# Performance work log

Measured on AMD Instinct MI355X. Metric: run time of the kernel, lower is better.

The kernel has to match this reference:

```python
import jax, jax.numpy as jnp
import numpy as np

NODE_DIM = 64
HIDDEN_DIM = 128
N_NODES = 100000
N_EDGES = 1000000


def setup_inputs() -> dict:
    key = jax.random.key(0)
    ks = jax.random.split(key, 9)
    node_rep = jax.random.normal(ks[0], (N_NODES, NODE_DIM), dtype=jnp.float32)
    edge_index = jax.random.randint(ks[1], (2, N_EDGES), 0, N_NODES, dtype=jnp.int64)
    s = 0.02  # init std (n_layers scale omitted; values irrelevant for math)
    W1 = jax.random.normal(ks[2], (2 * NODE_DIM, HIDDEN_DIM), dtype=jnp.float32) * s
    b1 = jnp.zeros((HIDDEN_DIM,), dtype=jnp.float32)
    W2 = jax.random.normal(ks[3], (HIDDEN_DIM, HIDDEN_DIM), dtype=jnp.float32) * s
    b2 = jnp.zeros((HIDDEN_DIM,), dtype=jnp.float32)
    W3 = jax.random.normal(ks[4], (HIDDEN_DIM, 1), dtype=jnp.float32) * s
    b3 = jnp.zeros((1,), dtype=jnp.float32)
    return {"node_rep": node_rep, "edge_index": edge_index,
            "W1": W1, "b1": b1, "W2": W2, "b2": b2, "W3": W3, "b3": b3}


def reference(node_rep, edge_index, W1, b1, W2, b2, W3, b3):
    # gather src/dst node reps per edge: [E, node_dim] each
    src = node_rep[edge_index[0]]
    dst = node_rep[edge_index[1]]
    feat = jnp.concatenate([src, dst], axis=-1)  # [E, 2*node_dim]
    h = jax.nn.relu(feat @ W1 + b1)              # [E, hidden]
    h = jax.nn.relu(h @ W2 + b2)                 # [E, hidden]
    logits = h @ W3 + b3                         # [E, 1]
    return jax.nn.sigmoid(jnp.squeeze(logits, axis=-1))  # [E]
```

## Files before the change

### kernel.cpp

```cpp
#include <hip/hip_runtime.h>
#include <math.h>

typedef float f32x16 __attribute__((ext_vector_type(16)));
typedef unsigned u32x4 __attribute__((ext_vector_type(4)));
typedef unsigned u32x2 __attribute__((ext_vector_type(2)));

#define N_NODES 100000
#define N_EDGESC 1000000
#define NODE_DIM 64
#define NG 31250
#define GPB 16
#define WBYTES 36864
#define BLOB (WBYTES + 512)

__device__ __forceinline__ unsigned pk2_lo(float a, float b){
#if __has_builtin(__builtin_amdgcn_cvt_pk_fp8_f32)
  return (unsigned)__builtin_amdgcn_cvt_pk_fp8_f32(a, b, 0, false);
#else
  unsigned r = 0;
  asm("v_cvt_pk_fp8_f32 %0, %1, %2" : "+v"(r) : "v"(a), "v"(b));
  return r;
#endif
}
__device__ __forceinline__ unsigned pk2_hi(float a, float b, unsigned old){
#if __has_builtin(__builtin_amdgcn_cvt_pk_fp8_f32)
  return (unsigned)__builtin_amdgcn_cvt_pk_fp8_f32(a, b, (int)old, true);
#else
  asm("v_cvt_pk_fp8_f32 %0, %1, %2 op_sel:[0,0,1]" : "+v"(old) : "v"(a), "v"(b));
  return old;
#endif
}
__device__ __forceinline__ unsigned pk4_fp8(float a, float b, float c, float d){
  return pk2_hi(c, d, pk2_lo(a, b));
}

__device__ __forceinline__ long pack64(unsigned lo, unsigned hi){
  return (long)(((unsigned long long)hi << 32) | lo);
}

__global__ void prep_kernel(const float* __restrict__ node,
                            const float* __restrict__ w1,
                            const float* __restrict__ w2,
                            const float* __restrict__ b1,
                            const float* __restrict__ b2,
                            const float* __restrict__ w3,
                            unsigned* __restrict__ nodef,
                            unsigned short* __restrict__ wfp,
                            float* __restrict__ w3s){
  const int b = blockIdx.x;
  if (b < 2048){
    int i = b * 256 + threadIdx.x;
    const int n4 = N_NODES * NODE_DIM / 4;
    const int stride = 2048 * 256;
    for (; i < n4; i += stride){
      const float4 v = reinterpret_cast<const float4*>(node)[i];
      nodef[i] = pk4_fp8(v.x, v.y, v.z, v.w);
    }
  } else {
    const int i = (b - 2048) * 256 + threadIdx.x;
    if (i < 18432){
      const int bi = i * 2;
      const int layer = (bi >= 18432);
      const int off = bi - (layer ? 18432 : 0);
      const int f = off >> 9, rem = off & 511, l = rem >> 3, j0 = rem & 7;
      const int kf = f >> 2, nt = f & 3;
      const int h = l >> 5, n = nt * 32 + (l & 31);
      float v0, v1;
      if (kf < 8){
        if (!layer){
          const int feat = (kf >> 2) * 64 + h * 32 + (kf & 3) * 8 + j0;
          v0 = 32.0f * w1[feat * 128 + n];
          v1 = 32.0f * w1[(feat + 1) * 128 + n];
        } else {
          const int k = kf * 16 + h * 8 + j0;
          v0 = 32.0f * w2[k * 128 + n];
          v1 = 32.0f * w2[(k + 1) * 128 + n];
        }
      } else {
        v0 = (h == 0 && j0 == 0) ? (layer ? 64.0f * b2[n] : 2.0f * b1[n]) : 0.0f;
        v1 = 0.0f;
      }
      wfp[i] = (unsigned short)(pk2_lo(v0, v1) & 0xffffu);
    } else if (i < 18432 + 128){
      const int c = i - 18432;
      w3s[c] = w3[c] * 0.0009765625f;
    }
  }
}

__device__ __forceinline__ void gather_fp8(const unsigned char* __restrict__ nodef,
                                           int is, int id, int h, u32x4 (&r)[4]){
  const unsigned char* s = nodef + (size_t)is * 64 + h * 32;
  const unsigned char* d = nodef + (size_t)id * 64 + h * 32;
  r[0] = *reinterpret_cast<const u32x4*>(s);
  r[1] = *reinterpret_cast<const u32x4*>(s + 16);
  r[2] = *reinterpret_cast<const u32x4*>(d);
  r[3] = *reinterpret_cast<const u32x4*>(d + 16);
}

template<bool PF>
__device__ __forceinline__ void do_pass(
    const unsigned char* wlds, int lane, int h, int er,
    u32x4 (&gA)[4], u32x4 (&gB)[4], long g0, bool v0, bool v1,
    const unsigned char* __restrict__ nodef, const int* __restrict__ eidx,
    long gn0, float bias3, float* __restrict__ out)
{
  int isAn = 0, idAn = 0, isBn = 0, idBn = 0;
  if (PF){
    const long ga = (gn0 < NG) ? gn0 : 0;
    const long gb = (gn0 + 1 < NG) ? gn0 + 1 : 0;
    isAn = eidx[ga * 32 + er];
    idAn = eidx[N_EDGESC + ga * 32 + er];
    isBn = eidx[gb * 32 + er];
    idBn = eidx[N_EDGESC + gb * 32 + er];
  }

  const long bbias = (h == 0) ? 0x58L : 0L;

  f32x16 acc[2][4];
  #pragma unroll
  for (int gi = 0; gi < 2; ++gi)
    #pragma unroll
    for (int nt = 0; nt < 4; ++nt)
      #pragma unroll
      for (int q = 0; q < 16; ++q) acc[gi][nt][q] = 0.f;

  __builtin_amdgcn_s_setprio(1);
  #pragma unroll
  for (int kf = 0; kf < 8; ++kf){
    const int dw = (kf >> 2) * 8 + (kf & 3) * 2;
    const long bA = pack64(gA[dw >> 2][dw & 3], gA[(dw + 1) >> 2][(dw + 1) & 3]);
    const long bB = pack64(gB[dw >> 2][dw & 3], gB[(dw + 1) >> 2][(dw + 1) & 3]);
    #pragma unroll
    for (int nt = 0; nt < 4; ++nt){
      const u32x2 av = *reinterpret_cast<const u32x2*>(wlds + (kf * 4 + nt) * 512 + lane * 8);
      const long a = pack64(av[0], av[1]);
      acc[0][nt] = __builtin_amdgcn_mfma_f32_32x32x16_fp8_fp8(a, bA, acc[0][nt], 0, 0, 0);
      acc[1][nt] = __builtin_amdgcn_mfma_f32_32x32x16_fp8_fp8(a, bB, acc[1][nt], 0, 0, 0);
    }
  }
  #pragma unroll
  for (int nt = 0; nt < 4; ++nt){
    const u32x2 av = *reinterpret_cast<const u32x2*>(wlds + (32 + nt) * 512 + lane * 8);
    const long a = pack64(av[0], av[1]);
    acc[0][nt] = __builtin_amdgcn_mfma_f32_32x32x16_fp8_fp8(a, bbias, acc[0][nt], 0, 0, 0);
    acc[1][nt] = __builtin_amdgcn_mfma_f32_32x32x16_fp8_fp8(a, bbias, acc[1][nt], 0, 0, 0);
  }
  __builtin_amdgcn_s_setprio(0);

  if (PF){
    gather_fp8(nodef, isAn, idAn, h, gA);
    gather_fp8(nodef, isBn, idBn, h, gB);
  }

  #pragma unroll
  for (int gi = 0; gi < 2; ++gi)
    #pragma unroll
    for (int nt = 0; nt < 4; ++nt)
      #pragma unroll
      for (int q = 0; q < 16; ++q)
        acc[gi][nt][q] = fmaxf(acc[gi][nt][q], 0.f);

  u32x2 b2fA[8], b2fB[8];
  #pragma unroll
  for (int gi = 0; gi < 2; ++gi){
    u32x2* b2f = gi ? b2fB : b2fA;
    #pragma unroll
    for (int nt = 0; nt < 4; ++nt){
      const unsigned u0 = pk4_fp8(acc[gi][nt][0],  acc[gi][nt][1],  acc[gi][nt][2],  acc[gi][nt][3]);
      const unsigned u1 = pk4_fp8(acc[gi][nt][4],  acc[gi][nt][5],  acc[gi][nt][6],  acc[gi][nt][7]);
      const unsigned u2 = pk4_fp8(acc[gi][nt][8],  acc[gi][nt][9],  acc[gi][nt][10], acc[gi][nt][11]);
      const unsigned u3 = pk4_fp8(acc[gi][nt][12], acc[gi][nt][13], acc[gi][nt][14], acc[gi][nt][15]);
      const unsigned s0 = h ? u0 : u1;
      const unsigned s1 = h ? u2 : u3;
      const unsigned t0 = (unsigned)__shfl_xor((int)s0, 32);
      const unsigned t1 = (unsigned)__shfl_xor((int)s1, 32);
      u32x2 f0, f1;
      f0[0] = h ? t0 : u0;  f0[1] = h ? u1 : t0;
      f1[0] = h ? t1 : u2;  f1[1] = h ? u3 : t1;
      b2f[2*nt]     = f0;
      b2f[2*nt + 1] = f1;
    }
  }

  #pragma unroll
  for (int gi = 0; gi < 2; ++gi)
    #pragma unroll
    for (int nt = 0; nt < 4; ++nt)
      #pragma unroll
      for (int q = 0; q < 16; ++q) acc[gi][nt][q] = 0.f;
  __builtin_amdgcn_s_setprio(1);
  #pragma unroll
  for (int kf = 0; kf < 8; ++kf){
    const long bA = pack64(b2fA[kf][0], b2fA[kf][1]);
    const long bB = pack64(b2fB[kf][0], b2fB[kf][1]);
    #pragma unroll
    for (int nt = 0; nt < 4; ++nt){
      const u32x2 av = *reinterpret_cast<const u32x2*>(wlds + 18432 + (kf * 4 + nt) * 512 + lane * 8);
      const long a = pack64(av[0], av[1]);
      acc[0][nt] = __builtin_amdgcn_mfma_f32_32x32x16_fp8_fp8(a, bA, acc[0][nt], 0, 0, 0);
      acc[1][nt] = __builtin_amdgcn_mfma_f32_32x32x16_fp8_fp8(a, bB, acc[1][nt], 0, 0, 0);
    }
  }
  #pragma unroll
  for (int nt = 0; nt < 4; ++nt){
    const u32x2 av = *reinterpret_cast<const u32x2*>(wlds + 18432 + (32 + nt) * 512 + lane * 8);
    const long a = pack64(av[0], av[1]);
    acc[0][nt] = __builtin_amdgcn_mfma_f32_32x32x16_fp8_fp8(a, bbias, acc[0][nt], 0, 0, 0);
    acc[1][nt] = __builtin_amdgcn_mfma_f32_32x32x16_fp8_fp8(a, bbias, acc[1][nt], 0, 0, 0);
  }
  __builtin_amdgcn_s_setprio(0);

  #pragma unroll
  for (int gi = 0; gi < 2; ++gi){
    float pv = 0.f;
    #pragma unroll
    for (int nt = 0; nt < 4; ++nt)
      #pragma unroll
      for (int rq = 0; rq < 4; ++rq){
        const int cb = nt * 32 + rq * 8 + 4 * h;
        const float4 ww = *reinterpret_cast<const float4*>(wlds + WBYTES + cb * 4);
        pv += fmaxf(acc[gi][nt][rq*4+0], 0.f) * ww.x;
        pv += fmaxf(acc[gi][nt][rq*4+1], 0.f) * ww.y;
        pv += fmaxf(acc[gi][nt][rq*4+2], 0.f) * ww.z;
        pv += fmaxf(acc[gi][nt][rq*4+3], 0.f) * ww.w;
      }
    pv += __shfl_xor(pv, 32);
    const long g = g0 + gi;
    const bool v = gi ? v1 : v0;
    if (h == 0 && v){
      out[g * 32 + er] = 1.f / (1.f + expf(-(pv + bias3)));
    }
  }
}

__global__ __launch_bounds__(256, 2) void mlp_main(
    const int* __restrict__ eidx,
    const unsigned char* __restrict__ nodef,
    const unsigned char* __restrict__ wblob,
    const float* __restrict__ b3,
    float* __restrict__ out)
{
  __shared__ unsigned char wlds[BLOB];

  const int tid  = threadIdx.x;
  const int wave = tid >> 6;
  const int lane = tid & 63;
  const int er   = lane & 31;
  const int h    = lane >> 5;

  const long g0 = (long)blockIdx.x * GPB + wave * 2;
  const long g1 = g0 + 8;
  const bool p0v0 = (g0 < NG), p0v1 = (g0 + 1 < NG);
  const bool p1v0 = (g1 < NG), p1v1 = (g1 + 1 < NG);

  u32x4 gA[4], gB[4];
  {
    const long ga = p0v0 ? g0 : 0;
    const long gb = p0v1 ? g0 + 1 : 0;
    const int isA = eidx[ga * 32 + er];
    const int idA = eidx[N_EDGESC + ga * 32 + er];
    const int isB = eidx[gb * 32 + er];
    const int idB = eidx[N_EDGESC + gb * 32 + er];
    gather_fp8(nodef, isA, idA, h, gA);
    gather_fp8(nodef, isB, idB, h, gB);
  }

  #pragma unroll
  for (int j = 0; j < 10; ++j){
    const int c = j * 256 + tid;
    if (c < BLOB / 16)
      reinterpret_cast<int4*>(wlds)[c] = reinterpret_cast<const int4*>(wblob)[c];
  }
  __syncthreads();

  const float bias3 = b3[0];

  do_pass<true >(wlds, lane, h, er, gA, gB, g0, p0v0, p0v1,
                 nodef, eidx, g1, bias3, out);
  do_pass<false>(wlds, lane, h, er, gA, gB, g1, p1v0, p1v1,
                 nodef, eidx, 0, bias3, out);
}

extern "C" void kernel_launch(void* const* d_in, const int* in_sizes, int n_in,
                              void* d_out, int out_size, void* d_ws, size_t ws_size,
                              hipStream_t stream){
  const float* node_rep = (const float*)d_in[0];
  const int*   eidx     = (const int*)d_in[1];
  const float* W1 = (const float*)d_in[2];
  const float* b1 = (const float*)d_in[3];
  const float* W2 = (const float*)d_in[4];
  const float* b2 = (const float*)d_in[5];
  const float* W3 = (const float*)d_in[6];
  const float* b3 = (const float*)d_in[7];
  float* out = (float*)d_out;

  unsigned* nodef = (unsigned*)d_ws;
  unsigned char* wblob = (unsigned char*)d_ws + (size_t)N_NODES * NODE_DIM;
  unsigned short* wfp = (unsigned short*)wblob;
  float* w3s = (float*)(wblob + WBYTES);

  prep_kernel<<<2048 + 128, 256, 0, stream>>>(node_rep, W1, W2, b1, b2, W3,
                                              nodef, wfp, w3s);

  const int nblocks = (NG + GPB - 1) / GPB;
  mlp_main<<<nblocks, 256, 0, stream>>>(eidx, (const unsigned char*)nodef,
                                        wblob, b3, out);
}
```

Baseline: 146.9 us.

## Process one edge group per wave per pass to raise occupancy

Each wave now handles a single 32-edge group per pass instead of two. That halves the accumulator and gather registers, which allows launch bounds of 3 blocks per CU instead of 2. GPB drops to 8, so the grid doubles and each block stages the LDS weights for fewer edges. The trade-off is less MFMA interleaving per wave and more repeated weight loads per edge, in exchange for more waves to hide gather latency.

```diff
diff --git a/kernel.cpp b/kernel.cpp
--- a/kernel.cpp
+++ b/kernel.cpp
@@ -9,7 +9,7 @@
 #define N_EDGESC 1000000
 #define NODE_DIM 64
 #define NG 31250
-#define GPB 16
+#define GPB 8
 #define WBYTES 36864
 #define BLOB (WBYTES + 512)
 
@@ -101,140 +101,109 @@
 template<bool PF>
 __device__ __forceinline__ void do_pass(
     const unsigned char* wlds, int lane, int h, int er,
-    u32x4 (&gA)[4], u32x4 (&gB)[4], long g0, bool v0, bool v1,
+    u32x4 (&gr)[4], long g, bool valid,
     const unsigned char* __restrict__ nodef, const int* __restrict__ eidx,
-    long gn0, float bias3, float* __restrict__ out)
+    long gn, float bias3, float* __restrict__ out)
 {
-  int isAn = 0, idAn = 0, isBn = 0, idBn = 0;
+  int isn = 0, idn = 0;
   if (PF){
-    const long ga = (gn0 < NG) ? gn0 : 0;
-    const long gb = (gn0 + 1 < NG) ? gn0 + 1 : 0;
-    isAn = eidx[ga * 32 + er];
-    idAn = eidx[N_EDGESC + ga * 32 + er];
-    isBn = eidx[gb * 32 + er];
-    idBn = eidx[N_EDGESC + gb * 32 + er];
+    const long gc = (gn < NG) ? gn : 0;
+    isn = eidx[gc * 32 + er];
+    idn = eidx[N_EDGESC + gc * 32 + er];
   }
 
   const long bbias = (h == 0) ? 0x58L : 0L;
 
-  f32x16 acc[2][4];
-  #pragma unroll
-  for (int gi = 0; gi < 2; ++gi)
-    #pragma unroll
-    for (int nt = 0; nt < 4; ++nt)
-      #pragma unroll
-      for (int q = 0; q < 16; ++q) acc[gi][nt][q] = 0.f;
+  f32x16 acc[4];
+  #pragma unroll
+  for (int nt = 0; nt < 4; ++nt)
+    #pragma unroll
+    for (int q = 0; q < 16; ++q) acc[nt][q] = 0.f;
 
   __builtin_amdgcn_s_setprio(1);
   #pragma unroll
   for (int kf = 0; kf < 8; ++kf){
     const int dw = (kf >> 2) * 8 + (kf & 3) * 2;
-    const long bA = pack64(gA[dw >> 2][dw & 3], gA[(dw + 1) >> 2][(dw + 1) & 3]);
-    const long bB = pack64(gB[dw >> 2][dw & 3], gB[(dw + 1) >> 2][(dw + 1) & 3]);
+    const long bfr = pack64(gr[dw >> 2][dw & 3], gr[(dw + 1) >> 2][(dw + 1) & 3]);
     #pragma unroll
     for (int nt = 0; nt < 4; ++nt){
       const u32x2 av = *reinterpret_cast<const u32x2*>(wlds + (kf * 4 + nt) * 512 + lane * 8);
-      const long a = pack64(av[0], av[1]);
-      acc[0][nt] = __builtin_amdgcn_mfma_f32_32x32x16_fp8_fp8(a, bA, acc[0][nt], 0, 0, 0);
-      acc[1][nt] = __builtin_amdgcn_mfma_f32_32x32x16_fp8_fp8(a, bB, acc[1][nt], 0, 0, 0);
+      acc[nt] = __builtin_amdgcn_mfma_f32_32x32x16_fp8_fp8(
+          pack64(av[0], av[1]), bfr, acc[nt], 0, 0, 0);
     }
   }
   #pragma unroll
   for (int nt = 0; nt < 4; ++nt){
     const u32x2 av = *reinterpret_cast<const u32x2*>(wlds + (32 + nt) * 512 + lane * 8);
-    const long a = pack64(av[0], av[1]);
-    acc[0][nt] = __builtin_amdgcn_mfma_f32_32x32x16_fp8_fp8(a, bbias, acc[0][nt], 0, 0, 0);
-    acc[1][nt] = __builtin_amdgcn_mfma_f32_32x32x16_fp8_fp8(a, bbias, acc[1][nt], 0, 0, 0);
+    acc[nt] = __builtin_amdgcn_mfma_f32_32x32x16_fp8_fp8(
+        pack64(av[0], av[1]), bbias, acc[nt], 0, 0, 0);
   }
   __builtin_amdgcn_s_setprio(0);
 
-  if (PF){
-    gather_fp8(nodef, isAn, idAn, h, gA);
-    gather_fp8(nodef, isBn, idBn, h, gB);
-  }
-
-  #pragma unroll
-  for (int gi = 0; gi < 2; ++gi)
-    #pragma unroll
-    for (int nt = 0; nt < 4; ++nt)
-      #pragma unroll
-      for (int q = 0; q < 16; ++q)
-        acc[gi][nt][q] = fmaxf(acc[gi][nt][q], 0.f);
-
-  u32x2 b2fA[8], b2fB[8];
-  #pragma unroll
-  for (int gi = 0; gi < 2; ++gi){
-    u32x2* b2f = gi ? b2fB : b2fA;
-    #pragma unroll
-    for (int nt = 0; nt < 4; ++nt){
-      const unsigned u0 = pk4_fp8(acc[gi][nt][0],  acc[gi][nt][1],  acc[gi][nt][2],  acc[gi][nt][3]);
-      const unsigned u1 = pk4_fp8(acc[gi][nt][4],  acc[gi][nt][5],  acc[gi][nt][6],  acc[gi][nt][7]);
-      const unsigned u2 = pk4_fp8(acc[gi][nt][8],  acc[gi][nt][9],  acc[gi][nt][10], acc[gi][nt][11]);
-      const unsigned u3 = pk4_fp8(acc[gi][nt][12], acc[gi][nt][13], acc[gi][nt][14], acc[gi][nt][15]);
-      const unsigned s0 = h ? u0 : u1;
-      const unsigned s1 = h ? u2 : u3;
-      const unsigned t0 = (unsigned)__shfl_xor((int)s0, 32);
-      const unsigned t1 = (unsigned)__shfl_xor((int)s1, 32);
-      u32x2 f0, f1;
-      f0[0] = h ? t0 : u0;  f0[1] = h ? u1 : t0;
-      f1[0] = h ? t1 : u2;  f1[1] = h ? u3 : t1;
-      b2f[2*nt]     = f0;
-      b2f[2*nt + 1] = f1;
-    }
-  }
-
-  #pragma unroll
-  for (int gi = 0; gi < 2; ++gi)
-    #pragma unroll
-    for (int nt = 0; nt < 4; ++nt)
-      #pragma unroll
-      for (int q = 0; q < 16; ++q) acc[gi][nt][q] = 0.f;
+  if (PF) gather_fp8(nodef, isn, idn, h, gr);
+
+  u32x2 b2f[8];
+  #pragma unroll
+  for (int nt = 0; nt < 4; ++nt){
+    #pragma unroll
+    for (int q = 0; q < 16; ++q) acc[nt][q] = fmaxf(acc[nt][q], 0.f);
+    const unsigned u0 = pk4_fp8(acc[nt][0],  acc[nt][1],  acc[nt][2],  acc[nt][3]);
+    const unsigned u1 = pk4_fp8(acc[nt][4],  acc[nt][5],  acc[nt][6],  acc[nt][7]);
+    const unsigned u2 = pk4_fp8(acc[nt][8],  acc[nt][9],  acc[nt][10], acc[nt][11]);
+    const unsigned u3 = pk4_fp8(acc[nt][12], acc[nt][13], acc[nt][14], acc[nt][15]);
+    const unsigned s0 = h ? u0 : u1;
+    const unsigned s1 = h ? u2 : u3;
+    const unsigned t0 = (unsigned)__shfl_xor((int)s0, 32);
+    const unsigned t1 = (unsigned)__shfl_xor((int)s1, 32);
+    u32x2 f0, f1;
+    f0[0] = h ? t0 : u0;  f0[1] = h ? u1 : t0;
+    f1[0] = h ? t1 : u2;  f1[1] = h ? u3 : t1;
+    b2f[2*nt]     = f0;
+    b2f[2*nt + 1] = f1;
+  }
+
+  #pragma unroll
+  for (int nt = 0; nt < 4; ++nt)
+    #pragma unroll
+    for (int q = 0; q < 16; ++q) acc[nt][q] = 0.f;
   __builtin_amdgcn_s_setprio(1);
   #pragma unroll
   for (int kf = 0; kf < 8; ++kf){
-    const long bA = pack64(b2fA[kf][0], b2fA[kf][1]);
-    const long bB = pack64(b2fB[kf][0], b2fB[kf][1]);
+    const long bfr = pack64(b2f[kf][0], b2f[kf][1]);
     #pragma unroll
     for (int nt = 0; nt < 4; ++nt){
       const u32x2 av = *reinterpret_cast<const u32x2*>(wlds + 18432 + (kf * 4 + nt) * 512 + lane * 8);
-      const long a = pack64(av[0], av[1]);
-      acc[0][nt] = __builtin_amdgcn_mfma_f32_32x32x16_fp8_fp8(a, bA, acc[0][nt], 0, 0, 0);
-      acc[1][nt] = __builtin_amdgcn_mfma_f32_32x32x16_fp8_fp8(a, bB, acc[1][nt], 0, 0, 0);
+      acc[nt] = __builtin_amdgcn_mfma_f32_32x32x16_fp8_fp8(
+          pack64(av[0], av[1]), bfr, acc[nt], 0, 0, 0);
     }
   }
   #pragma unroll
   for (int nt = 0; nt < 4; ++nt){
     const u32x2 av = *reinterpret_cast<const u32x2*>(wlds + 18432 + (32 + nt) * 512 + lane * 8);
-    const long a = pack64(av[0], av[1]);
-    acc[0][nt] = __builtin_amdgcn_mfma_f32_32x32x16_fp8_fp8(a, bbias, acc[0][nt], 0, 0, 0);
-    acc[1][nt] = __builtin_amdgcn_mfma_f32_32x32x16_fp8_fp8(a, bbias, acc[1][nt], 0, 0, 0);
+    acc[nt] = __builtin_amdgcn_mfma_f32_32x32x16_fp8_fp8(
+        pack64(av[0], av[1]), bbias, acc[nt], 0, 0, 0);
   }
   __builtin_amdgcn_s_setprio(0);
 
-  #pragma unroll
-  for (int gi = 0; gi < 2; ++gi){
-    float pv = 0.f;
-    #pragma unroll
-    for (int nt = 0; nt < 4; ++nt)
-      #pragma unroll
-      for (int rq = 0; rq < 4; ++rq){
-        const int cb = nt * 32 + rq * 8 + 4 * h;
-        const float4 ww = *reinterpret_cast<const float4*>(wlds + WBYTES + cb * 4);
-        pv += fmaxf(acc[gi][nt][rq*4+0], 0.f) * ww.x;
-        pv += fmaxf(acc[gi][nt][rq*4+1], 0.f) * ww.y;
-        pv += fmaxf(acc[gi][nt][rq*4+2], 0.f) * ww.z;
-        pv += fmaxf(acc[gi][nt][rq*4+3], 0.f) * ww.w;
-      }
-    pv += __shfl_xor(pv, 32);
-    const long g = g0 + gi;
-    const bool v = gi ? v1 : v0;
-    if (h == 0 && v){
-      out[g * 32 + er] = 1.f / (1.f + expf(-(pv + bias3)));
-    }
-  }
-}
-
-__global__ __launch_bounds__(256, 2) void mlp_main(
+  float pv = 0.f;
+  #pragma unroll
+  for (int nt = 0; nt < 4; ++nt)
+    #pragma unroll
+    for (int rq = 0; rq < 4; ++rq){
+      const int cb = nt * 32 + rq * 8 + 4 * h;
+      const float4 ww = *reinterpret_cast<const float4*>(wlds + WBYTES + cb * 4);
+      pv += fmaxf(acc[nt][rq*4+0], 0.f) * ww.x;
+      pv += fmaxf(acc[nt][rq*4+1], 0.f) * ww.y;
+      pv += fmaxf(acc[nt][rq*4+2], 0.f) * ww.z;
+      pv += fmaxf(acc[nt][rq*4+3], 0.f) * ww.w;
+    }
+  pv += __shfl_xor(pv, 32);
+  if (h == 0 && valid){
+    out[g * 32 + er] = 1.f / (1.f + expf(-(pv + bias3)));
+  }
+}
+
+__global__ __launch_bounds__(256, 3) void mlp_main(
     const int* __restrict__ eidx,
     const unsigned char* __restrict__ nodef,
     const unsigned char* __restrict__ wblob,
@@ -249,21 +218,16 @@
   const int er   = lane & 31;
   const int h    = lane >> 5;
 
-  const long g0 = (long)blockIdx.x * GPB + wave * 2;
-  const long g1 = g0 + 8;
-  const bool p0v0 = (g0 < NG), p0v1 = (g0 + 1 < NG);
-  const bool p1v0 = (g1 < NG), p1v1 = (g1 + 1 < NG);
-
-  u32x4 gA[4], gB[4];
+  const long g0 = (long)blockIdx.x * GPB + wave;
+  const long g1 = g0 + 4;
+  const bool v0 = (g0 < NG), v1 = (g1 < NG);
+
+  u32x4 gr[4];
   {
-    const long ga = p0v0 ? g0 : 0;
-    const long gb = p0v1 ? g0 + 1 : 0;
-    const int isA = eidx[ga * 32 + er];
-    const int idA = eidx[N_EDGESC + ga * 32 + er];
-    const int isB = eidx[gb * 32 + er];
-    const int idB = eidx[N_EDGESC + gb * 32 + er];
-    gather_fp8(nodef, isA, idA, h, gA);
-    gather_fp8(nodef, isB, idB, h, gB);
+    const long gc = v0 ? g0 : 0;
+    const int is = eidx[gc * 32 + er];
+    const int id = eidx[N_EDGESC + gc * 32 + er];
+    gather_fp8(nodef, is, id, h, gr);
   }
 
   #pragma unroll
@@ -276,10 +240,8 @@
 
   const float bias3 = b3[0];
 
-  do_pass<true >(wlds, lane, h, er, gA, gB, g0, p0v0, p0v1,
-                 nodef, eidx, g1, bias3, out);
-  do_pass<false>(wlds, lane, h, er, gA, gB, g1, p1v0, p1v1,
-                 nodef, eidx, 0, bias3, out);
+  do_pass<true >(wlds, lane, h, er, gr, g0, v0, nodef, eidx, g1, bias3, out);
+  do_pass<false>(wlds, lane, h, er, gr, g1, v1, nodef, eidx, 0,  bias3, out);
 }
 
 extern "C" void kernel_launch(void* const* d_in, const int* in_sizes, int n_in,
```

New measurement: 142.2 us. 1.03x faster.
